# Performance work log

Hardware: AMD Instinct MI355X
Metric: run time of the kernel (lower is better)

Reference implementation:

```python
import jax, jax.numpy as jnp
import numpy as np

B, N, M = 2, 2048, 1024
C, CTX, H = 1024, 1024, 16
D = C // H
HID = int(C * 4.0)
EPS = 1e-6


def _ln(h):
    # LayerNorm32: fp32 layernorm, eps=1e-6, no affine params
    h32 = h.astype(jnp.float32)
    mu = jnp.mean(h32, axis=-1, keepdims=True)
    var = jnp.var(h32, axis=-1, keepdims=True)
    return ((h32 - mu) * jax.lax.rsqrt(var + EPS)).astype(h.dtype)


def _sdpa(q, k, v):
    # q: [B,Q,H,D], k/v: [B,K,H,D]
    scale = 1.0 / np.sqrt(D)
    s = jnp.einsum('bqhd,bkhd->bhqk', q, k) * scale
    p = jax.nn.softmax(s, axis=-1)
    return jnp.einsum('bhqk,bkhd->bqhd', p, v)


def _forward(x, context, Wqkv, bqkv, Wos, bos, Wq, bq, Wkv, bkv, Woc, boc, W1, b1, W2, b2):
    Bx, Nx, _ = x.shape
    Mx = context.shape[1]
    # --- self-attention (attn_mode='full') ---
    h = _ln(x)
    qkv = (h @ Wqkv + bqkv).reshape(Bx, Nx, 3, H, D)
    q, k, v = qkv[:, :, 0], qkv[:, :, 1], qkv[:, :, 2]
    a = _sdpa(q, k, v).reshape(Bx, Nx, C)
    x = x + (a @ Wos + bos)
    # --- cross-attention (always 'full') ---
    h = _ln(x)
    q = (h @ Wq + bq).reshape(Bx, Nx, H, D)
    kv = (context @ Wkv + bkv).reshape(Bx, Mx, 2, H, D)
    k, v = kv[:, :, 0], kv[:, :, 1]
    a = _sdpa(q, k, v).reshape(Bx, Nx, C)
    x = x + (a @ Woc + boc)
    # --- FFN with tanh-approx GELU ---
    h = _ln(x)
    x = x + (jax.nn.gelu(h @ W1 + b1, approximate=True) @ W2 + b2)
    return x


def setup_inputs() -> dict:
    key = jax.random.key(0)
    ks = jax.random.split(key, 12)
    rn = lambda k, shape: (jax.random.normal(k, shape, jnp.float32) * 0.02)
    return {
        'x': jax.random.normal(ks[0], (B, N, C), jnp.float32),
        'context': jax.random.normal(ks[1], (B, M, CTX), jnp.float32),
        'Wqkv': rn(ks[2], (C, 3 * C)), 'bqkv': jnp.zeros((3 * C,), jnp.float32),
        'Wos': rn(ks[3], (C, C)), 'bos': jnp.zeros((C,), jnp.float32),
        'Wq': rn(ks[4], (C, C)), 'bq': jnp.zeros((C,), jnp.float32),
        'Wkv': rn(ks[5], (CTX, 2 * C)), 'bkv': jnp.zeros((2 * C,), jnp.float32),
        'Woc': rn(ks[6], (C, C)), 'boc': jnp.zeros((C,), jnp.float32),
        'W1': rn(ks[7], (C, HID)), 'b1': jnp.zeros((HID,), jnp.float32),
        'W2': rn(ks[8], (HID, C)), 'b2': jnp.zeros((C,), jnp.float32),
    }


def reference(x, context, Wqkv, bqkv, Wos, bos, Wq, bq, Wkv, bkv, Woc, boc, W1, b1, W2, b2):
    return _forward(x, context, Wqkv, bqkv, Wos, bos, Wq, bq, Wkv, bkv, Woc, boc, W1, b1, W2, b2)
```

## Files before the change

kernel.cpp:

```cpp
#include <hip/hip_runtime.h>
#include <cstdint>

typedef unsigned short u16;
typedef short bf16x8 __attribute__((ext_vector_type(8)));
typedef unsigned short u16x8 __attribute__((ext_vector_type(8)));
typedef float f32x4 __attribute__((ext_vector_type(4)));

__device__ __forceinline__ u16 f2bf(float f) {
  union { float f; uint32_t u; } v; v.f = f;
  uint32_t r = (v.u + 0x7fffu + ((v.u >> 16) & 1u)) >> 16;
  return (u16)r;
}

__device__ __forceinline__ void gload_lds16(const u16* g, u16* l) {
  __builtin_amdgcn_global_load_lds(
      (const __attribute__((address_space(1))) void*)g,
      (__attribute__((address_space(3))) void*)l, 16, 0, 0);
}

__global__ __launch_bounds__(256) void ln_kernel(const float* __restrict__ x,
                                                 u16* __restrict__ h) {
  const int row = blockIdx.x;
  const int tid = threadIdx.x;
  const float4 v = *reinterpret_cast<const float4*>(x + (long)row * 1024 + tid * 4);
  float s  = v.x + v.y + v.z + v.w;
  float ss = v.x * v.x + v.y * v.y + v.z * v.z + v.w * v.w;
#pragma unroll
  for (int off = 32; off >= 1; off >>= 1) {
    s  += __shfl_xor(s, off, 64);
    ss += __shfl_xor(ss, off, 64);
  }
  __shared__ float red[8];
  const int wave = tid >> 6, lane = tid & 63;
  if (lane == 0) { red[wave] = s; red[4 + wave] = ss; }
  __syncthreads();
  s  = red[0] + red[1] + red[2] + red[3];
  ss = red[4] + red[5] + red[6] + red[7];
  const float mu   = s * (1.0f / 1024.0f);
  const float var  = ss * (1.0f / 1024.0f) - mu * mu;
  const float rstd = rsqrtf(var + 1e-6f);
  ushort4 o;
  o.x = f2bf((v.x - mu) * rstd);
  o.y = f2bf((v.y - mu) * rstd);
  o.z = f2bf((v.z - mu) * rstd);
  o.w = f2bf((v.w - mu) * rstd);
  *reinterpret_cast<ushort4*>(h + (long)row * 1024 + tid * 4) = o;
}

struct WEnt { const float* W; u16* Wt; int K, N, tEnd; };
struct WEnts { WEnt e[7]; int n; };

__global__ __launch_bounds__(256) void wconvert_all(WEnts args) {
  __shared__ u16 tile[64][72];
  int t = blockIdx.x;
  int i = 0, tStart = 0;
  while (i < args.n - 1 && t >= args.e[i].tEnd) { tStart = args.e[i].tEnd; i++; }
  const float* W = args.e[i].W;
  u16* Wt = args.e[i].Wt;
  const int K = args.e[i].K, N = args.e[i].N;
  const int rel = t - tStart;
  const int ntn = N >> 6;
  const int tn = rel % ntn, tk = rel / ntn;
  const int n0 = tn * 64, k0 = tk * 64;

  const int th = threadIdx.x;
  const int c4 = (th & 15) * 4;
  const int r  = th >> 4;
#pragma unroll
  for (int ii = 0; ii < 4; ii++) {
    const int row = ii * 16 + r;
    const float4 v = *reinterpret_cast<const float4*>(W + (long)(k0 + row) * N + n0 + c4);
    tile[c4 + 0][row] = f2bf(v.x);
    tile[c4 + 1][row] = f2bf(v.y);
    tile[c4 + 2][row] = f2bf(v.z);
    tile[c4 + 3][row] = f2bf(v.w);
  }
  __syncthreads();
  const int c8 = (th & 7) * 8;
  const int rn = th >> 3;
#pragma unroll
  for (int ii = 0; ii < 2; ii++) {
    const int row = ii * 32 + rn;
    *reinterpret_cast<u16x8*>(Wt + (long)(n0 + row) * K + k0 + c8) =
        *reinterpret_cast<const u16x8*>(&tile[row][c8]);
  }
}

__global__ __launch_bounds__(256) void f2bf_kernel(const float* __restrict__ in,
                                                   u16* __restrict__ out) {
  const long i = ((long)blockIdx.x * 256 + threadIdx.x) * 4;
  const float4 v = *reinterpret_cast<const float4*>(in + i);
  ushort4 o;
  o.x = f2bf(v.x); o.y = f2bf(v.y); o.z = f2bf(v.z); o.w = f2bf(v.w);
  *reinterpret_cast<ushort4*>(out + i) = o;
}

__global__ __launch_bounds__(256) void vtrans(const u16* __restrict__ V,
                                              u16* __restrict__ Vt,
                                              int vStride, long vBatch, int nk) {
  __shared__ u16 tile[64][72];
  const int t = threadIdx.x;
  const int b = blockIdx.z, h = blockIdx.y, n0 = blockIdx.x * 64;
  const u16* vp = V + (long)b * vBatch + h * 64;
  u16* op = Vt + (long)(b * 16 + h) * 64 * (long)nk + n0;
  const int ch = t & 7;
#pragma unroll
  for (int i = 0; i < 2; i++) {
    const int n = (t >> 3) + i * 32;
    const u16x8 v = *reinterpret_cast<const u16x8*>(vp + (long)(n0 + n) * vStride + ch * 8);
#pragma unroll
    for (int j = 0; j < 8; j++) tile[ch * 8 + j][n] = v[j];
  }
  __syncthreads();
#pragma unroll
  for (int i = 0; i < 2; i++) {
    const int d = (t >> 3) + i * 32;
    *reinterpret_cast<u16x8*>(op + (long)d * nk + ch * 8) =
        *reinterpret_cast<const u16x8*>(&tile[d][ch * 8]);
  }
}

template <int TN, int SX, bool OUT_BF16, bool GELU_ACT, bool RES>
__global__ __launch_bounds__(256, 2) void gemm_bt(
    const u16* __restrict__ A, const u16* __restrict__ Bt,
    const float* __restrict__ bias, const float* __restrict__ res,
    void* __restrict__ Cout, int Ndim, int Kdim, int lx, int ly) {
  constexpr int NFRAG = TN / 32;
  __shared__ u16 Al[2][128 * 32];
  __shared__ u16 Bl[2][TN * 32];
  const int j = blockIdx.x;
  const int c = j & 7, kk = j >> 3;
  const int cx = c % SX, cy = c / SX;
  const int bx = cx * lx + (kk % lx);
  const int by = cy * ly + (kk / lx);
  const int m0 = by * 128, n0 = bx * TN;

  const int tid  = threadIdx.x;
  const int lane = tid & 63, wave = tid >> 6;
  const int quad = lane >> 4, l15 = lane & 15;
  const int wr = wave >> 1, wc = wave & 1;

  f32x4 acc[4][NFRAG];
  const f32x4 vzero = {0.f, 0.f, 0.f, 0.f};
#pragma unroll
  for (int i = 0; i < 4; i++)
#pragma unroll
    for (int jj = 0; jj < NFRAG; jj++) acc[i][jj] = vzero;

  const long rowOff = (long)(lane >> 2) * Kdim + (lane & 3) * 8;
  const u16* gA = A  + (long)m0 * Kdim + rowOff;
  const u16* gB = Bt + (long)n0 * Kdim + rowOff;

  auto stage = [&](int k0, int p) {
    gload_lds16(gA + (long)(wave * 16) * Kdim + k0,       &Al[p][wave * 512]);
    gload_lds16(gA + (long)((wave + 4) * 16) * Kdim + k0, &Al[p][(wave + 4) * 512]);
    gload_lds16(gB + (long)(wave * 16) * Kdim + k0,       &Bl[p][wave * 512]);
    if constexpr (TN == 128)
      gload_lds16(gB + (long)((wave + 4) * 16) * Kdim + k0, &Bl[p][(wave + 4) * 512]);
  };

  stage(0, 0);
  int p = 0;
  for (int k0 = 0; k0 < Kdim; k0 += 32, p ^= 1) {
    __syncthreads();
    bf16x8 af[4], bfr[NFRAG];
#pragma unroll
    for (int mt = 0; mt < 4; mt++)
      af[mt] = *reinterpret_cast<const bf16x8*>(&Al[p][(wr * 64 + mt * 16 + l15) * 32 + quad * 8]);
#pragma unroll
    for (int nt = 0; nt < NFRAG; nt++)
      bfr[nt] = *reinterpret_cast<const bf16x8*>(&Bl[p][(wc * NFRAG * 16 + nt * 16 + l15) * 32 + quad * 8]);
    if (k0 + 32 < Kdim) stage(k0 + 32, p ^ 1);
#pragma unroll
    for (int mt = 0; mt < 4; mt++)
#pragma unroll
      for (int nt = 0; nt < NFRAG; nt++)
        acc[mt][nt] = __builtin_amdgcn_mfma_f32_16x16x32_bf16(af[mt], bfr[nt], acc[mt][nt], 0, 0, 0);
  }

#pragma unroll
  for (int nt = 0; nt < NFRAG; nt++) {
    const int col = n0 + wc * NFRAG * 16 + nt * 16 + l15;
    const float bv = bias[col];
#pragma unroll
    for (int mt = 0; mt < 4; mt++) {
#pragma unroll
      for (int r = 0; r < 4; r++) {
        const int row = m0 + wr * 64 + mt * 16 + quad * 4 + r;
        float y = acc[mt][nt][r] + bv;
        if (GELU_ACT) {
          const float t = 0.7978845608028654f * (y + 0.044715f * y * y * y);
          y = 0.5f * y * (1.0f + tanhf(t));
        }
        if (RES) y += res[(long)row * Ndim + col];
        if (OUT_BF16)
          ((u16*)Cout)[(long)row * Ndim + col] = f2bf(y);
        else
          ((float*)Cout)[(long)row * Ndim + col] = y;
      }
    }
  }
}

__global__ __launch_bounds__(256, 2) void attn_kernel(
    const u16* __restrict__ Q, const u16* __restrict__ K, const u16* __restrict__ Vt,
    u16* __restrict__ O, int nk, int qStride, int kStride, int oStride,
    long qBatch, long kBatch, long oBatch) {
  __shared__ u16 Kt[2][64 * 64];
  __shared__ u16 Vl[2][64 * 64];
  __shared__ u16 Pl[4][32 * 64];

  const int tid = threadIdx.x;
  const int lane = tid & 63, wave = tid >> 6;
  const int quad = lane >> 4, l15 = lane & 15;
  const int b = blockIdx.z, hh = blockIdx.y, qt = blockIdx.x;

  const u16* qp = Q + (long)b * qBatch + hh * 64;
  const u16* kp = K + (long)b * kBatch + hh * 64;
  const u16* vp = Vt + (long)(b * 16 + hh) * 64 * (long)nk;

  bf16x8 qf[2][2];
  const int qrow = qt * 128 + wave * 32 + l15;
#pragma unroll
  for (int qg = 0; qg < 2; qg++) {
    qf[qg][0] = *reinterpret_cast<const bf16x8*>(qp + (long)(qrow + qg * 16) * qStride + quad * 8);
    qf[qg][1] = *reinterpret_cast<const bf16x8*>(qp + (long)(qrow + qg * 16) * qStride + 32 + quad * 8);
  }

  const int r8 = lane >> 3;
  const int gcol = ((lane & 7) ^ r8) * 8;
  const u16* kgA = kp + (long)(wave * 8 + r8) * kStride + gcol;
  const u16* kgB = kp + (long)((wave + 4) * 8 + r8) * kStride + gcol;
  const u16* vgA = vp + (long)(wave * 8 + r8) * nk + gcol;
  const u16* vgB = vp + (long)((wave + 4) * 8 + r8) * nk + gcol;

  const int cF = (quad ^ (l15 & 7)) * 8;

  const f32x4 vzero = {0.f, 0.f, 0.f, 0.f};
  f32x4 oAcc[2][4];
  float lSt[2] = {0.f, 0.f};
#pragma unroll
  for (int qg = 0; qg < 2; qg++)
#pragma unroll
    for (int i = 0; i < 4; i++) oAcc[qg][i] = vzero;

  const float SCL = 0.18033688f;
  const int nTiles = nk >> 6;
  const long kAdv = (long)64 * kStride;

  auto stage = [&](int kt, int p) {
    gload_lds16(kgA + kt * kAdv, &Kt[p][wave * 512]);
    gload_lds16(kgB + kt * kAdv, &Kt[p][(wave + 4) * 512]);
    gload_lds16(vgA + kt * 64,   &Vl[p][wave * 512]);
    gload_lds16(vgB + kt * 64,   &Vl[p][(wave + 4) * 512]);
  };

  stage(0, 0);
  int p = 0;
  for (int kt = 0; kt < nTiles; kt++, p ^= 1) {
    __syncthreads();
    if (kt + 1 < nTiles) stage(kt + 1, p ^ 1);

    f32x4 st[2][4];
#pragma unroll
    for (int mt = 0; mt < 4; mt++) {
      const bf16x8 kf0 = *reinterpret_cast<const bf16x8*>(&Kt[p][(mt * 16 + l15) * 64 + cF]);
      const bf16x8 kf1 = *reinterpret_cast<const bf16x8*>(&Kt[p][(mt * 16 + l15) * 64 + (cF ^ 32)]);
#pragma unroll
      for (int qg = 0; qg < 2; qg++) {
        f32x4 z = vzero;
        z = __builtin_amdgcn_mfma_f32_16x16x32_bf16(kf0, qf[qg][0], z, 0, 0, 0);
        z = __builtin_amdgcn_mfma_f32_16x16x32_bf16(kf1, qf[qg][1], z, 0, 0, 0);
        st[qg][mt] = z;
      }
    }

#pragma unroll
    for (int qg = 0; qg < 2; qg++) {
      float ps = 0.f;
#pragma unroll
      for (int mt = 0; mt < 4; mt++)
#pragma unroll
        for (int r = 0; r < 4; r++) {
          const float pw = __builtin_amdgcn_exp2f(st[qg][mt][r] * SCL);
          st[qg][mt][r] = pw;
          ps += pw;
        }
      lSt[qg] += ps;
      u16* plw = &Pl[wave][(qg * 16 + l15) * 64];
#pragma unroll
      for (int mt = 0; mt < 4; mt++) {
        union { float f; uint32_t u; } a0, a1, a2, a3;
        a0.f = st[qg][mt][0]; a1.f = st[qg][mt][1];
        a2.f = st[qg][mt][2]; a3.f = st[qg][mt][3];
        a0.u += 0x8000u; a1.u += 0x8000u; a2.u += 0x8000u; a3.u += 0x8000u;
        uint2 w;
        w.x = __builtin_amdgcn_perm(a1.u, a0.u, 0x07060302u);
        w.y = __builtin_amdgcn_perm(a3.u, a2.u, 0x07060302u);
        const int pcol = (((mt * 2 + (quad >> 1)) ^ (l15 & 7)) * 8) + (quad & 1) * 4;
        *reinterpret_cast<uint2*>(&plw[pcol]) = w;
      }
    }

    bf16x8 pf[2][2];
#pragma unroll
    for (int qg = 0; qg < 2; qg++) {
      const u16* plw = &Pl[wave][(qg * 16 + l15) * 64];
      pf[qg][0] = *reinterpret_cast<const bf16x8*>(&plw[cF]);
      pf[qg][1] = *reinterpret_cast<const bf16x8*>(&plw[cF ^ 32]);
    }
#pragma unroll
    for (int dt = 0; dt < 4; dt++) {
      const bf16x8 vf0 = *reinterpret_cast<const bf16x8*>(&Vl[p][(dt * 16 + l15) * 64 + cF]);
      const bf16x8 vf1 = *reinterpret_cast<const bf16x8*>(&Vl[p][(dt * 16 + l15) * 64 + (cF ^ 32)]);
#pragma unroll
      for (int qg = 0; qg < 2; qg++) {
        oAcc[qg][dt] = __builtin_amdgcn_mfma_f32_16x16x32_bf16(pf[qg][0], vf0, oAcc[qg][dt], 0, 0, 0);
        oAcc[qg][dt] = __builtin_amdgcn_mfma_f32_16x16x32_bf16(pf[qg][1], vf1, oAcc[qg][dt], 0, 0, 0);
      }
    }
  }

  u16* op = O + (long)b * oBatch + hh * 64;
#pragma unroll
  for (int qg = 0; qg < 2; qg++) {
    float l = lSt[qg];
    l += __shfl_xor(l, 16, 64);
    l += __shfl_xor(l, 32, 64);
    float lR[4];
#pragma unroll
    for (int r = 0; r < 4; r++) lR[r] = 1.0f / __shfl(l, quad * 4 + r, 64);
#pragma unroll
    for (int dt = 0; dt < 4; dt++)
#pragma unroll
      for (int r = 0; r < 4; r++) {
        const int row = qt * 128 + wave * 32 + qg * 16 + quad * 4 + r;
        op[(long)row * oStride + dt * 16 + l15] = f2bf(oAcc[qg][dt][r] * lR[r]);
      }
  }
}

extern "C" void kernel_launch(void* const* d_in, const int* in_sizes, int n_in,
                              void* d_out, int out_size, void* d_ws, size_t ws_size,
                              hipStream_t stream) {
  const float* x    = (const float*)d_in[0];
  const float* ctx  = (const float*)d_in[1];
  const float* Wqkv = (const float*)d_in[2];
  const float* bqkv = (const float*)d_in[3];
  const float* Wos  = (const float*)d_in[4];
  const float* bos  = (const float*)d_in[5];
  const float* Wq   = (const float*)d_in[6];
  const float* bq   = (const float*)d_in[7];
  const float* Wkv  = (const float*)d_in[8];
  const float* bkv  = (const float*)d_in[9];
  const float* Woc  = (const float*)d_in[10];
  const float* boc  = (const float*)d_in[11];
  const float* W1   = (const float*)d_in[12];
  const float* b1   = (const float*)d_in[13];
  const float* W2   = (const float*)d_in[14];
  const float* b2   = (const float*)d_in[15];
  float* out = (float*)d_out;
  char* ws = (char*)d_ws;
  const size_t MB = 1024 * 1024;

  if (ws_size >= 80 * MB) {
    u16* Wqkvt = (u16*)(ws + 0 * MB);
    u16* Wost  = (u16*)(ws + 6 * MB);
    u16* Wqt   = (u16*)(ws + 8 * MB);
    u16* Wkvt  = (u16*)(ws + 10 * MB);
    u16* Woct  = (u16*)(ws + 14 * MB);
    u16* W1t   = (u16*)(ws + 16 * MB);
    u16* W2t   = (u16*)(ws + 24 * MB);
    u16* h     = (u16*)(ws + 32 * MB);
    u16* abuf  = (u16*)(ws + 40 * MB);
    u16* qkv   = (u16*)(ws + 48 * MB);
    u16* q2    = (u16*)(ws + 48 * MB);
    u16* kv2   = (u16*)(ws + 56 * MB);
    u16* ctxbf = (u16*)(ws + 64 * MB);
    u16* VtCr  = (u16*)(ws + 68 * MB);
    u16* hid   = (u16*)(ws + 48 * MB);
    u16* VtSelf = h;

    WEnts we;
    we.n = 7;
    we.e[0] = {Wqkv, Wqkvt, 1024, 3072, 768};
    we.e[1] = {Wos,  Wost,  1024, 1024, 1024};
    we.e[2] = {Wq,   Wqt,   1024, 1024, 1280};
    we.e[3] = {Wkv,  Wkvt,  1024, 2048, 1792};
    we.e[4] = {Woc,  Woct,  1024, 1024, 2048};
    we.e[5] = {W1,   W1t,   1024, 4096, 3072};
    we.e[6] = {W2,   W2t,   4096, 1024, 4096};
    wconvert_all<<<dim3(4096), dim3(256), 0, stream>>>(we);
    f2bf_kernel<<<dim3(2048), dim3(256), 0, stream>>>(ctx, ctxbf);

    ln_kernel<<<dim3(4096), dim3(256), 0, stream>>>(x, h);
    gemm_bt<128, 2, true, false, false><<<dim3(768), dim3(256), 0, stream>>>(
        h, Wqkvt, bqkv, nullptr, qkv, 3072, 1024, 12, 8);
    vtrans<<<dim3(32, 16, 2), dim3(256), 0, stream>>>(
        qkv + 2048, VtSelf, 3072, (long)2048 * 3072, 2048);
    attn_kernel<<<dim3(16, 16, 2), dim3(256), 0, stream>>>(
        qkv, qkv + 1024, VtSelf, abuf, 2048, 3072, 3072, 1024,
        (long)2048 * 3072, (long)2048 * 3072, (long)2048 * 1024);
    gemm_bt<64, 1, false, false, true><<<dim3(512), dim3(256), 0, stream>>>(
        abuf, Wost, bos, x, out, 1024, 1024, 16, 4);
    ln_kernel<<<dim3(4096), dim3(256), 0, stream>>>(out, h);
    gemm_bt<64, 1, true, false, false><<<dim3(512), dim3(256), 0, stream>>>(
        h, Wqt, bq, nullptr, q2, 1024, 1024, 16, 4);
    gemm_bt<64, 2, true, false, false><<<dim3(512), dim3(256), 0, stream>>>(
        ctxbf, Wkvt, bkv, nullptr, kv2, 2048, 1024, 16, 4);
    vtrans<<<dim3(16, 16, 2), dim3(256), 0, stream>>>(
        kv2 + 1024, VtCr, 2048, (long)1024 * 2048, 1024);
    attn_kernel<<<dim3(16, 16, 2), dim3(256), 0, stream>>>(
        q2, kv2, VtCr, abuf, 1024, 1024, 2048, 1024,
        (long)2048 * 1024, (long)1024 * 2048, (long)2048 * 1024);
    gemm_bt<64, 1, false, false, true><<<dim3(512), dim3(256), 0, stream>>>(
        abuf, Woct, boc, out, out, 1024, 1024, 16, 4);
    ln_kernel<<<dim3(4096), dim3(256), 0, stream>>>(out, h);
    gemm_bt<128, 2, true, true, false><<<dim3(1024), dim3(256), 0, stream>>>(
        h, W1t, b1, nullptr, hid, 4096, 1024, 16, 8);
    gemm_bt<128, 2, false, false, true><<<dim3(256), dim3(256), 0, stream>>>(
        hid, W2t, b2, out, out, 1024, 4096, 4, 8);
  } else {
    u16* h      = (u16*)ws;
    u16* wbuf   = (u16*)(ws + 8 * MB);
    char* C0    = ws + 16 * MB;
    u16* qkv    = (u16*)C0;
    u16* Wqkvt  = (u16*)(C0 + 24 * MB);
    u16* Wost   = (u16*)C0;
    u16* q2     = (u16*)C0;
    u16* kv2    = (u16*)(C0 + 8 * MB);
    u16* Wqt    = (u16*)(C0 + 16 * MB);
    u16* Wkvt   = (u16*)(C0 + 16 * MB);
    u16* ctxbf  = (u16*)(C0 + 20 * MB);
    u16* VtCr   = (u16*)(C0 + 24 * MB);
    u16* Woct   = (u16*)(C0 + 16 * MB);
    u16* hid    = (u16*)C0;
    u16* VtSelf = h;
    u16* abuf   = wbuf;
    u16* W1t    = wbuf;
    u16* W2t    = wbuf;
    WEnts w1; w1.n = 1;

    ln_kernel<<<dim3(4096), dim3(256), 0, stream>>>(x, h);
    w1.e[0] = {Wqkv, Wqkvt, 1024, 3072, 768};
    wconvert_all<<<dim3(768), dim3(256), 0, stream>>>(w1);
    gemm_bt<128, 2, true, false, false><<<dim3(768), dim3(256), 0, stream>>>(
        h, Wqkvt, bqkv, nullptr, qkv, 3072, 1024, 12, 8);
    vtrans<<<dim3(32, 16, 2), dim3(256), 0, stream>>>(
        qkv + 2048, VtSelf, 3072, (long)2048 * 3072, 2048);
    attn_kernel<<<dim3(16, 16, 2), dim3(256), 0, stream>>>(
        qkv, qkv + 1024, VtSelf, abuf, 2048, 3072, 3072, 1024,
        (long)2048 * 3072, (long)2048 * 3072, (long)2048 * 1024);
    w1.e[0] = {Wos, Wost, 1024, 1024, 256};
    wconvert_all<<<dim3(256), dim3(256), 0, stream>>>(w1);
    gemm_bt<64, 1, false, false, true><<<dim3(512), dim3(256), 0, stream>>>(
        abuf, Wost, bos, x, out, 1024, 1024, 16, 4);
    ln_kernel<<<dim3(4096), dim3(256), 0, stream>>>(out, h);
    w1.e[0] = {Wq, Wqt, 1024, 1024, 256};
    wconvert_all<<<dim3(256), dim3(256), 0, stream>>>(w1);
    gemm_bt<64, 1, true, false, false><<<dim3(512), dim3(256), 0, stream>>>(
        h, Wqt, bq, nullptr, q2, 1024, 1024, 16, 4);
    f2bf_kernel<<<dim3(2048), dim3(256), 0, stream>>>(ctx, ctxbf);
    w1.e[0] = {Wkv, Wkvt, 1024, 2048, 512};
    wconvert_all<<<dim3(512), dim3(256), 0, stream>>>(w1);
    gemm_bt<64, 2, true, false, false><<<dim3(512), dim3(256), 0, stream>>>(
        ctxbf, Wkvt, bkv, nullptr, kv2, 2048, 1024, 16, 4);
    vtrans<<<dim3(16, 16, 2), dim3(256), 0, stream>>>(
        kv2 + 1024, VtCr, 2048, (long)1024 * 2048, 1024);
    attn_kernel<<<dim3(16, 16, 2), dim3(256), 0, stream>>>(
        q2, kv2, VtCr, abuf, 1024, 1024, 2048, 1024,
        (long)2048 * 1024, (long)1024 * 2048, (long)2048 * 1024);
    w1.e[0] = {Woc, Woct, 1024, 1024, 256};
    wconvert_all<<<dim3(256), dim3(256), 0, stream>>>(w1);
    gemm_bt<64, 1, false, false, true><<<dim3(512), dim3(256), 0, stream>>>(
        abuf, Woct, boc, out, out, 1024, 1024, 16, 4);
    ln_kernel<<<dim3(4096), dim3(256), 0, stream>>>(out, h);
    w1.e[0] = {W1, W1t, 1024, 4096, 1024};
    wconvert_all<<<dim3(1024), dim3(256), 0, stream>>>(w1);
    gemm_bt<128, 2, true, true, false><<<dim3(1024), dim3(256), 0, stream>>>(
        h, W1t, b1, nullptr, hid, 4096, 1024, 16, 8);
    w1.e[0] = {W2, W2t, 4096, 1024, 1024};
    wconvert_all<<<dim3(1024), dim3(256), 0, stream>>>(w1);
    gemm_bt<128, 2, false, false, true><<<dim3(256), dim3(256), 0, stream>>>(
        hid, W2t, b2, out, out, 1024, 4096, 4, 8);
  }
}
```

Measured before the change: 492.7 us.

## Split-K the W2 FFN GEMM with atomics and swizzle LDS reads

The final FFN down-projection GEMM (K=4096, only 256 blocks) is split in two along K across blockIdx.y, and each half atomically adds its partial sums into the output, which already holds the residual. This doubles the block count to fill more CUs. Separately, all gemm_bt instances now XOR-swizzle the 16-byte chunk placement in LDS on load and read, to cut bank conflicts on fragment reads. Atomic float adds make the summation order nondeterministic, and the residual add now depends on out already holding x.

```diff
diff --git a/kernel.cpp b/kernel.cpp
--- a/kernel.cpp
+++ b/kernel.cpp
@@ -120,7 +120,7 @@
   }
 }
 
-template <int TN, int SX, bool OUT_BF16, bool GELU_ACT, bool RES>
+template <int TN, int SX, bool OUT_BF16, bool GELU_ACT, bool RES, bool SPLITK = false>
 __global__ __launch_bounds__(256, 2) void gemm_bt(
     const u16* __restrict__ A, const u16* __restrict__ Bt,
     const float* __restrict__ bias, const float* __restrict__ res,
@@ -147,9 +147,12 @@
 #pragma unroll
     for (int jj = 0; jj < NFRAG; jj++) acc[i][jj] = vzero;
 
-  const long rowOff = (long)(lane >> 2) * Kdim + (lane & 3) * 8;
-  const u16* gA = A  + (long)m0 * Kdim + rowOff;
-  const u16* gB = Bt + (long)n0 * Kdim + rowOff;
+  const int Keff = SPLITK ? (Kdim >> 1) : Kdim;
+  const long kOff = SPLITK ? (long)blockIdx.y * Keff : 0;
+
+  const long rowOff = (long)(lane >> 2) * Kdim + (((lane & 3) ^ ((lane >> 3) & 3)) * 8);
+  const u16* gA = A  + (long)m0 * Kdim + rowOff + kOff;
+  const u16* gB = Bt + (long)n0 * Kdim + rowOff + kOff;
 
   auto stage = [&](int k0, int p) {
     gload_lds16(gA + (long)(wave * 16) * Kdim + k0,       &Al[p][wave * 512]);
@@ -159,18 +162,20 @@
       gload_lds16(gB + (long)((wave + 4) * 16) * Kdim + k0, &Bl[p][(wave + 4) * 512]);
   };
 
+  const int swz = (quad ^ ((l15 >> 1) & 3)) * 8;
+
   stage(0, 0);
   int p = 0;
-  for (int k0 = 0; k0 < Kdim; k0 += 32, p ^= 1) {
+  for (int k0 = 0; k0 < Keff; k0 += 32, p ^= 1) {
     __syncthreads();
     bf16x8 af[4], bfr[NFRAG];
 #pragma unroll
     for (int mt = 0; mt < 4; mt++)
-      af[mt] = *reinterpret_cast<const bf16x8*>(&Al[p][(wr * 64 + mt * 16 + l15) * 32 + quad * 8]);
+      af[mt] = *reinterpret_cast<const bf16x8*>(&Al[p][(wr * 64 + mt * 16 + l15) * 32 + swz]);
 #pragma unroll
     for (int nt = 0; nt < NFRAG; nt++)
-      bfr[nt] = *reinterpret_cast<const bf16x8*>(&Bl[p][(wc * NFRAG * 16 + nt * 16 + l15) * 32 + quad * 8]);
-    if (k0 + 32 < Kdim) stage(k0 + 32, p ^ 1);
+      bfr[nt] = *reinterpret_cast<const bf16x8*>(&Bl[p][(wc * NFRAG * 16 + nt * 16 + l15) * 32 + swz]);
+    if (k0 + 32 < Keff) stage(k0 + 32, p ^ 1);
 #pragma unroll
     for (int mt = 0; mt < 4; mt++)
 #pragma unroll
@@ -187,16 +192,22 @@
 #pragma unroll
       for (int r = 0; r < 4; r++) {
         const int row = m0 + wr * 64 + mt * 16 + quad * 4 + r;
-        float y = acc[mt][nt][r] + bv;
-        if (GELU_ACT) {
-          const float t = 0.7978845608028654f * (y + 0.044715f * y * y * y);
-          y = 0.5f * y * (1.0f + tanhf(t));
+        if constexpr (SPLITK) {
+          float y = acc[mt][nt][r];
+          if (blockIdx.y == 0) y += bv;
+          unsafeAtomicAdd(&((float*)Cout)[(long)row * Ndim + col], y);
+        } else {
+          float y = acc[mt][nt][r] + bv;
+          if (GELU_ACT) {
+            const float t = 0.7978845608028654f * (y + 0.044715f * y * y * y);
+            y = 0.5f * y * (1.0f + tanhf(t));
+          }
+          if (RES) y += res[(long)row * Ndim + col];
+          if (OUT_BF16)
+            ((u16*)Cout)[(long)row * Ndim + col] = f2bf(y);
+          else
+            ((float*)Cout)[(long)row * Ndim + col] = y;
         }
-        if (RES) y += res[(long)row * Ndim + col];
-        if (OUT_BF16)
-          ((u16*)Cout)[(long)row * Ndim + col] = f2bf(y);
-        else
-          ((float*)Cout)[(long)row * Ndim + col] = y;
       }
     }
   }
@@ -418,8 +429,8 @@
     ln_kernel<<<dim3(4096), dim3(256), 0, stream>>>(out, h);
     gemm_bt<128, 2, true, true, false><<<dim3(1024), dim3(256), 0, stream>>>(
         h, W1t, b1, nullptr, hid, 4096, 1024, 16, 8);
-    gemm_bt<128, 2, false, false, true><<<dim3(256), dim3(256), 0, stream>>>(
-        hid, W2t, b2, out, out, 1024, 4096, 4, 8);
+    gemm_bt<128, 2, false, false, false, true><<<dim3(256, 2), dim3(256), 0, stream>>>(
+        hid, W2t, b2, nullptr, out, 1024, 4096, 4, 8);
   } else {
     u16* h      = (u16*)ws;
     u16* wbuf   = (u16*)(ws + 8 * MB);
@@ -481,7 +492,7 @@
         h, W1t, b1, nullptr, hid, 4096, 1024, 16, 8);
     w1.e[0] = {W2, W2t, 4096, 1024, 1024};
     wconvert_all<<<dim3(1024), dim3(256), 0, stream>>>(w1);
-    gemm_bt<128, 2, false, false, true><<<dim3(256), dim3(256), 0, stream>>>(
-        hid, W2t, b2, out, out, 1024, 4096, 4, 8);
-  }
-}
+    gemm_bt<128, 2, false, false, false, true><<<dim3(256, 2), dim3(256), 0, stream>>>(
+        hid, W2t, b2, nullptr, out, 1024, 4096, 4, 8);
+  }
+}
```

Measured after the change: 482.4 us. -2.1%, faster.
